# Optimization experiments

Measured on AMD Instinct MI355X. Metric: run time of the kernel, lower is better.

The kernel has to match this reference:

```python
import jax, jax.numpy as jnp
import numpy as np

N = 100000      # number of target nodes
K = 6           # num_sample + self
V = 200000      # feature table rows
D = 128         # feature dim

def setup_inputs() -> dict:
    key = jax.random.key(0)
    k1, k2 = jax.random.split(key)
    features = jax.random.normal(k1, (V, D), dtype=jnp.float32)
    neigh_idx = jax.random.randint(k2, (N, K), 0, V, dtype=jnp.int64)
    return {"features": features, "neigh_idx": neigh_idx}

def reference(features, neigh_idx):
    # Equivalent of mask.div(num_neigh).mm(embed_matrix):
    # gather each node's (sampled + self) neighbor rows and take the mean.
    # [N, K, D] gather -> mean over K -> [N, D]
    gathered = jnp.take(features, neigh_idx, axis=0)
    return gathered.mean(axis=1)
```

## Files before the change

### kernel.cpp

```cpp
#include <hip/hip_runtime.h>


#define K_NEIGH 6
#define D_FEAT 128
#define NODES_PER_BLOCK 8

__global__ __launch_bounds__(256) void MeanAggregator_16415365005349_kernel(
    const float* __restrict__ feat,
    const int* __restrict__ idx,
    float* __restrict__ out,
    int N) {
  const int node = blockIdx.x * NODES_PER_BLOCK + (threadIdx.x >> 5);
  const int lane = threadIdx.x & 31;
  if (node >= N) return;

  int r[K_NEIGH];
#pragma unroll
  for (int k = 0; k < K_NEIGH; ++k) r[k] = idx[(size_t)node * K_NEIGH + k];

  float4 v[K_NEIGH];
#pragma unroll
  for (int k = 0; k < K_NEIGH; ++k) {
    const float4* row = reinterpret_cast<const float4*>(feat + (size_t)r[k] * D_FEAT);
    v[k] = row[lane];
  }

  float4 acc;
  acc.x = v[0].x; acc.y = v[0].y; acc.z = v[0].z; acc.w = v[0].w;
#pragma unroll
  for (int k = 1; k < K_NEIGH; ++k) {
    acc.x += v[k].x; acc.y += v[k].y; acc.z += v[k].z; acc.w += v[k].w;
  }
  const float s = 1.0f / (float)K_NEIGH;
  acc.x *= s; acc.y *= s; acc.z *= s; acc.w *= s;

  reinterpret_cast<float4*>(out + (size_t)node * D_FEAT)[lane] = acc;
}

extern "C" void kernel_launch(void* const* d_in, const int* in_sizes, int n_in,
                              void* d_out, int out_size, void* d_ws, size_t ws_size,
                              hipStream_t stream) {
  const float* feat = (const float*)d_in[0];
  const int* idx = (const int*)d_in[1];
  float* out = (float*)d_out;

  const int N = in_sizes[1] / K_NEIGH;
  const int blocks = (N + NODES_PER_BLOCK - 1) / NODES_PER_BLOCK;
  hipLaunchKernelGGL(MeanAggregator_16415365005349_kernel,
                     dim3(blocks), dim3(256), 0, stream,
                     feat, idx, out, N);
}
```

Before: 55.91 us.

## Use grid-stride loop with index prefetch and nontemporal output stores

Replaces one-node-per-warp blocks with a capped grid of 2048 blocks that loop over nodes with a grid stride. While the current node's feature rows are being gathered, the neighbor indices for the next node are loaded, hiding that dependent load latency. Output is written with nontemporal stores so streamed results do not pollute the cache. Capping the grid reduces how many gathers are in flight at once, which could cost memory-level parallelism on a latency-bound random gather.

Measured after the change: 56.83 us. Within noise of the previous version (+1.7%).

```diff
diff --git a/kernel.cpp b/kernel.cpp
--- a/kernel.cpp
+++ b/kernel.cpp
@@ -1,5 +1,7 @@
 #include <hip/hip_runtime.h>
 
+
+typedef float f32x4 __attribute__((ext_vector_type(4)));
 
 #define K_NEIGH 6
 #define D_FEAT 128
@@ -10,31 +12,45 @@
     const int* __restrict__ idx,
     float* __restrict__ out,
     int N) {
-  const int node = blockIdx.x * NODES_PER_BLOCK + (threadIdx.x >> 5);
+  const int slot = threadIdx.x >> 5;
   const int lane = threadIdx.x & 31;
-  if (node >= N) return;
+  const int stride = gridDim.x * NODES_PER_BLOCK;
+
+  int node = blockIdx.x * NODES_PER_BLOCK + slot;
 
   int r[K_NEIGH];
+  if (node < N) {
 #pragma unroll
-  for (int k = 0; k < K_NEIGH; ++k) r[k] = idx[(size_t)node * K_NEIGH + k];
-
-  float4 v[K_NEIGH];
-#pragma unroll
-  for (int k = 0; k < K_NEIGH; ++k) {
-    const float4* row = reinterpret_cast<const float4*>(feat + (size_t)r[k] * D_FEAT);
-    v[k] = row[lane];
+    for (int k = 0; k < K_NEIGH; ++k) r[k] = idx[(size_t)node * K_NEIGH + k];
   }
 
-  float4 acc;
-  acc.x = v[0].x; acc.y = v[0].y; acc.z = v[0].z; acc.w = v[0].w;
+  while (node < N) {
+    const int next = node + stride;
+
+    f32x4 v[K_NEIGH];
 #pragma unroll
-  for (int k = 1; k < K_NEIGH; ++k) {
-    acc.x += v[k].x; acc.y += v[k].y; acc.z += v[k].z; acc.w += v[k].w;
+    for (int k = 0; k < K_NEIGH; ++k) {
+      v[k] = reinterpret_cast<const f32x4*>(feat + (size_t)r[k] * D_FEAT)[lane];
+    }
+
+    int rn[K_NEIGH];
+    if (next < N) {
+#pragma unroll
+      for (int k = 0; k < K_NEIGH; ++k) rn[k] = idx[(size_t)next * K_NEIGH + k];
+    }
+
+    f32x4 acc = v[0];
+#pragma unroll
+    for (int k = 1; k < K_NEIGH; ++k) acc += v[k];
+    acc *= (1.0f / (float)K_NEIGH);
+
+    f32x4* dst = reinterpret_cast<f32x4*>(out + (size_t)node * D_FEAT) + lane;
+    __builtin_nontemporal_store(acc, dst);
+
+#pragma unroll
+    for (int k = 0; k < K_NEIGH; ++k) r[k] = rn[k];
+    node = next;
   }
-  const float s = 1.0f / (float)K_NEIGH;
-  acc.x *= s; acc.y *= s; acc.z *= s; acc.w *= s;
-
-  reinterpret_cast<float4*>(out + (size_t)node * D_FEAT)[lane] = acc;
 }
 
 extern "C" void kernel_launch(void* const* d_in, const int* in_sizes, int n_in,
@@ -45,7 +61,11 @@
   float* out = (float*)d_out;
 
   const int N = in_sizes[1] / K_NEIGH;
-  const int blocks = (N + NODES_PER_BLOCK - 1) / NODES_PER_BLOCK;
+
+  const int max_blocks = 2048;
+  int blocks = (N + NODES_PER_BLOCK - 1) / NODES_PER_BLOCK;
+  if (blocks > max_blocks) blocks = max_blocks;
+
   hipLaunchKernelGGL(MeanAggregator_16415365005349_kernel,
                      dim3(blocks), dim3(256), 0, stream,
                      feat, idx, out, N);
```
